# Kernel tuning notes

Measured on AMD Instinct MI355X. Metric: run time of the kernel, lower is better.

Reference implementation:

```python
import jax, jax.numpy as jnp
import numpy as np

B, IN_DIM, OUT_DIM = 4096, 8192, 8192

# Each of the 16 gates op_i(a,b) is affine in (1, a, b, a*b).
# Rows: [const, coef_a, coef_b, coef_ab] for gate i = 0..15.
GATE_COEF = np.array([
    [0.,  0.,  0.,  0.],   # 0: zeros
    [0.,  0.,  0.,  1.],   # 1: a*b
    [0.,  1.,  0., -1.],   # 2: a - a*b
    [0.,  1.,  0.,  0.],   # 3: a
    [0.,  0.,  1., -1.],   # 4: b - a*b
    [0.,  0.,  1.,  0.],   # 5: b
    [0.,  1.,  1., -2.],   # 6: a + b - 2ab (xor)
    [0.,  1.,  1., -1.],   # 7: a + b - ab (or)
    [1., -1., -1.,  1.],   # 8: 1 - (a + b - ab)
    [1., -1., -1.,  2.],   # 9: 1 - (a + b - 2ab)
    [1.,  0., -1.,  0.],   # 10: 1 - b
    [1.,  0., -1.,  1.],   # 11: 1 - b + ab
    [1., -1.,  0.,  0.],   # 12: 1 - a
    [1., -1.,  0.,  1.],   # 13: 1 - a + ab
    [1.,  0.,  0., -1.],   # 14: 1 - ab
    [1.,  0.,  0.,  0.],   # 15: ones
], dtype=np.float32)


def setup_inputs() -> dict:
    key = jax.random.key(0)
    k1, k2, k3, k4 = jax.random.split(key, 4)
    x = jax.random.uniform(k1, (B, IN_DIM), dtype=jnp.float32)
    weights = jax.random.normal(k2, (OUT_DIM, 16), dtype=jnp.float32)
    idx0 = jax.random.randint(k3, (OUT_DIM,), 0, IN_DIM)
    idx1 = jax.random.randint(k4, (OUT_DIM,), 0, IN_DIM)
    return {"x": x, "weights": weights, "idx0": idx0, "idx1": idx1}


def reference(x, weights, idx0, idx1):
    # training path: soft mixture over 16 gates
    p = jax.nn.softmax(weights, axis=-1)          # [out_dim, 16]
    c = p @ jnp.asarray(GATE_COEF)                # [out_dim, 4]: sum_i p_i * op_i collapsed
    a = x[:, idx0]                                # [B, out_dim]
    b = x[:, idx1]                                # [B, out_dim]
    return c[:, 0] + c[:, 1] * a + c[:, 2] * b + c[:, 3] * (a * b)
```

## Files before the change

kernel.cpp:

```cpp
#include <hip/hip_runtime.h>

#define IN_DIM 8192
#define OUT_DIM 8192
#define NROWS 4096
#define THREADS 512
#define JITERS (OUT_DIM / (THREADS * 4))

__device__ __constant__ float GATE_COEF[16][4] = {
    {0.f, 0.f, 0.f, 0.f}, {0.f, 0.f, 0.f, 1.f}, {0.f, 1.f, 0.f, -1.f}, {0.f, 1.f, 0.f, 0.f},
    {0.f, 0.f, 1.f, -1.f}, {0.f, 0.f, 1.f, 0.f}, {0.f, 1.f, 1.f, -2.f}, {0.f, 1.f, 1.f, -1.f},
    {1.f, -1.f, -1.f, 1.f}, {1.f, -1.f, -1.f, 2.f}, {1.f, 0.f, -1.f, 0.f}, {1.f, 0.f, -1.f, 1.f},
    {1.f, -1.f, 0.f, 0.f}, {1.f, -1.f, 0.f, 1.f}, {1.f, 0.f, 0.f, -1.f}, {1.f, 0.f, 0.f, 0.f}};

__global__ __launch_bounds__(256) void compute_c_kernel(const float* __restrict__ w,
                                                        float4* __restrict__ c) {
    int j = blockIdx.x * blockDim.x + threadIdx.x;
    if (j >= OUT_DIM) return;
    const float4* wv = (const float4*)(w + (size_t)j * 16);
    float4 w0 = wv[0], w1 = wv[1], w2 = wv[2], w3 = wv[3];
    float wa[16] = {w0.x, w0.y, w0.z, w0.w, w1.x, w1.y, w1.z, w1.w,
                    w2.x, w2.y, w2.z, w2.w, w3.x, w3.y, w3.z, w3.w};
    float m = wa[0];
#pragma unroll
    for (int k = 1; k < 16; ++k) m = fmaxf(m, wa[k]);
    float p[16];
    float s = 0.f;
#pragma unroll
    for (int k = 0; k < 16; ++k) {
        p[k] = __expf(wa[k] - m);
        s += p[k];
    }
    float inv = 1.f / s;
    float c0 = 0.f, c1 = 0.f, c2 = 0.f, c3 = 0.f;
#pragma unroll
    for (int k = 0; k < 16; ++k) {
        c0 = fmaf(p[k], GATE_COEF[k][0], c0);
        c1 = fmaf(p[k], GATE_COEF[k][1], c1);
        c2 = fmaf(p[k], GATE_COEF[k][2], c2);
        c3 = fmaf(p[k], GATE_COEF[k][3], c3);
    }
    c[j] = make_float4(c0 * inv, c1 * inv, c2 * inv, c3 * inv);
}

__global__ __launch_bounds__(THREADS, 8) void gate_kernel(const float* __restrict__ x,
                                                          const float4* __restrict__ c,
                                                          const int* __restrict__ idx0,
                                                          const int* __restrict__ idx1,
                                                          float* __restrict__ out) {
    __shared__ float row[IN_DIM];
    const int i = blockIdx.x;
    const int tid = threadIdx.x;
    const float4* xr = (const float4*)(x + (size_t)i * IN_DIM);
    float4* rowv = (float4*)row;

    float4 s0 = xr[tid];
    float4 s1 = xr[tid + THREADS];
    float4 s2 = xr[tid + 2 * THREADS];
    float4 s3 = xr[tid + 3 * THREADS];

    const int j0 = tid * 4;
    int4 pi0 = *(const int4*)(idx0 + j0);
    int4 pi1 = *(const int4*)(idx1 + j0);

    rowv[tid] = s0;
    rowv[tid + THREADS] = s1;
    rowv[tid + 2 * THREADS] = s2;
    rowv[tid + 3 * THREADS] = s3;
    __syncthreads();

    float* orow = out + (size_t)i * OUT_DIM;
#pragma unroll
    for (int k = 0; k < JITERS; ++k) {
        const int j = k * (THREADS * 4) + tid * 4;
        const int4 i0 = pi0;
        const int4 i1 = pi1;
        if (k < JITERS - 1) {
            const int jn = j + THREADS * 4;
            pi0 = *(const int4*)(idx0 + jn);
            pi1 = *(const int4*)(idx1 + jn);
        }
        const float4 ca = c[j + 0];
        const float4 cb = c[j + 1];
        const float4 cc = c[j + 2];
        const float4 cd = c[j + 3];
        float a, b;
        float4 o;
        a = row[i0.x]; b = row[i1.x];
        o.x = fmaf(a * b, ca.w, fmaf(b, ca.z, fmaf(a, ca.y, ca.x)));
        a = row[i0.y]; b = row[i1.y];
        o.y = fmaf(a * b, cb.w, fmaf(b, cb.z, fmaf(a, cb.y, cb.x)));
        a = row[i0.z]; b = row[i1.z];
        o.z = fmaf(a * b, cc.w, fmaf(b, cc.z, fmaf(a, cc.y, cc.x)));
        a = row[i0.w]; b = row[i1.w];
        o.w = fmaf(a * b, cd.w, fmaf(b, cd.z, fmaf(a, cd.y, cd.x)));
        *(float4*)(orow + j) = o;
    }
}

extern "C" void kernel_launch(void* const* d_in, const int* in_sizes, int n_in,
                              void* d_out, int out_size, void* d_ws, size_t ws_size,
                              hipStream_t stream) {
    const float* x = (const float*)d_in[0];
    const float* weights = (const float*)d_in[1];
    const int* idx0 = (const int*)d_in[2];
    const int* idx1 = (const int*)d_in[3];
    float* out = (float*)d_out;
    float4* c = (float4*)d_ws;

    compute_c_kernel<<<OUT_DIM / 256, 256, 0, stream>>>(weights, c);
    gate_kernel<<<NROWS, THREADS, 0, stream>>>(x, c, idx0, idx1, out);
}
```

Measured before the change: 277.6 us.

## Process two rows per block, use SoA coefficients and nontemporal loads/stores

Each block now stages two x rows in shared memory (64KB) and reuses the index and coefficient loads for both rows. The coefficients are stored structure-of-arrays so each thread reads four coalesced float4 vectors instead of four scattered float4 per output. Loads of x and stores of out use nontemporal hints to avoid polluting cache. The doubled LDS footprint lowers the number of resident blocks per CU, which may reduce latency hiding.

```diff
diff --git a/kernel.cpp b/kernel.cpp
--- a/kernel.cpp
+++ b/kernel.cpp
@@ -4,7 +4,10 @@
 #define OUT_DIM 8192
 #define NROWS 4096
 #define THREADS 512
+#define RPB 2
 #define JITERS (OUT_DIM / (THREADS * 4))
+
+typedef float v4f __attribute__((ext_vector_type(4)));
 
 __device__ __constant__ float GATE_COEF[16][4] = {
     {0.f, 0.f, 0.f, 0.f}, {0.f, 0.f, 0.f, 1.f}, {0.f, 1.f, 0.f, -1.f}, {0.f, 1.f, 0.f, 0.f},
@@ -13,7 +16,7 @@
     {1.f, -1.f, 0.f, 0.f}, {1.f, -1.f, 0.f, 1.f}, {1.f, 0.f, 0.f, -1.f}, {1.f, 0.f, 0.f, 0.f}};
 
 __global__ __launch_bounds__(256) void compute_c_kernel(const float* __restrict__ w,
-                                                        float4* __restrict__ c) {
+                                                        float* __restrict__ cp) {
     int j = blockIdx.x * blockDim.x + threadIdx.x;
     if (j >= OUT_DIM) return;
     const float4* wv = (const float4*)(w + (size_t)j * 16);
@@ -39,36 +42,48 @@
         c2 = fmaf(p[k], GATE_COEF[k][2], c2);
         c3 = fmaf(p[k], GATE_COEF[k][3], c3);
     }
-    c[j] = make_float4(c0 * inv, c1 * inv, c2 * inv, c3 * inv);
+    cp[j] = c0 * inv;
+    cp[j + OUT_DIM] = c1 * inv;
+    cp[j + 2 * OUT_DIM] = c2 * inv;
+    cp[j + 3 * OUT_DIM] = c3 * inv;
 }
 
-__global__ __launch_bounds__(THREADS, 8) void gate_kernel(const float* __restrict__ x,
-                                                          const float4* __restrict__ c,
+__global__ __launch_bounds__(THREADS, 4) void gate_kernel(const float* __restrict__ x,
+                                                          const float* __restrict__ cp,
                                                           const int* __restrict__ idx0,
                                                           const int* __restrict__ idx1,
                                                           float* __restrict__ out) {
-    __shared__ float row[IN_DIM];
-    const int i = blockIdx.x;
+    __shared__ float rows[RPB * IN_DIM];
+    const int r0 = blockIdx.x * RPB;
     const int tid = threadIdx.x;
-    const float4* xr = (const float4*)(x + (size_t)i * IN_DIM);
-    float4* rowv = (float4*)row;
 
-    float4 s0 = xr[tid];
-    float4 s1 = xr[tid + THREADS];
-    float4 s2 = xr[tid + 2 * THREADS];
-    float4 s3 = xr[tid + 3 * THREADS];
+    const v4f* xr0 = (const v4f*)(x + (size_t)r0 * IN_DIM);
+    const v4f* xr1 = (const v4f*)(x + (size_t)(r0 + 1) * IN_DIM);
+    v4f* rv0 = (v4f*)rows;
+    v4f* rv1 = (v4f*)(rows + IN_DIM);
+    v4f st[8];
+#pragma unroll
+    for (int t = 0; t < 4; ++t) st[t] = __builtin_nontemporal_load(xr0 + tid + t * THREADS);
+#pragma unroll
+    for (int t = 0; t < 4; ++t) st[4 + t] = __builtin_nontemporal_load(xr1 + tid + t * THREADS);
 
     const int j0 = tid * 4;
     int4 pi0 = *(const int4*)(idx0 + j0);
     int4 pi1 = *(const int4*)(idx1 + j0);
 
-    rowv[tid] = s0;
-    rowv[tid + THREADS] = s1;
-    rowv[tid + 2 * THREADS] = s2;
-    rowv[tid + 3 * THREADS] = s3;
+#pragma unroll
+    for (int t = 0; t < 4; ++t) rv0[tid + t * THREADS] = st[t];
+#pragma unroll
+    for (int t = 0; t < 4; ++t) rv1[tid + t * THREADS] = st[4 + t];
     __syncthreads();
 
-    float* orow = out + (size_t)i * OUT_DIM;
+    const float* __restrict__ c0p = cp;
+    const float* __restrict__ c1p = cp + OUT_DIM;
+    const float* __restrict__ c2p = cp + 2 * OUT_DIM;
+    const float* __restrict__ c3p = cp + 3 * OUT_DIM;
+    float* o0 = out + (size_t)r0 * OUT_DIM;
+    float* o1 = out + (size_t)(r0 + 1) * OUT_DIM;
+
 #pragma unroll
     for (int k = 0; k < JITERS; ++k) {
         const int j = k * (THREADS * 4) + tid * 4;
@@ -79,21 +94,22 @@
             pi0 = *(const int4*)(idx0 + jn);
             pi1 = *(const int4*)(idx1 + jn);
         }
-        const float4 ca = c[j + 0];
-        const float4 cb = c[j + 1];
-        const float4 cc = c[j + 2];
-        const float4 cd = c[j + 3];
-        float a, b;
-        float4 o;
-        a = row[i0.x]; b = row[i1.x];
-        o.x = fmaf(a * b, ca.w, fmaf(b, ca.z, fmaf(a, ca.y, ca.x)));
-        a = row[i0.y]; b = row[i1.y];
-        o.y = fmaf(a * b, cb.w, fmaf(b, cb.z, fmaf(a, cb.y, cb.x)));
-        a = row[i0.z]; b = row[i1.z];
-        o.z = fmaf(a * b, cc.w, fmaf(b, cc.z, fmaf(a, cc.y, cc.x)));
-        a = row[i0.w]; b = row[i1.w];
-        o.w = fmaf(a * b, cd.w, fmaf(b, cd.z, fmaf(a, cd.y, cd.x)));
-        *(float4*)(orow + j) = o;
+        const v4f c0v = *(const v4f*)(c0p + j);
+        const v4f c1v = *(const v4f*)(c1p + j);
+        const v4f c2v = *(const v4f*)(c2p + j);
+        const v4f c3v = *(const v4f*)(c3p + j);
+        v4f a0, b0, a1, b1;
+        a0.x = rows[i0.x]; a0.y = rows[i0.y]; a0.z = rows[i0.z]; a0.w = rows[i0.w];
+        b0.x = rows[i1.x]; b0.y = rows[i1.y]; b0.z = rows[i1.z]; b0.w = rows[i1.w];
+        a1.x = rows[IN_DIM + i0.x]; a1.y = rows[IN_DIM + i0.y];
+        a1.z = rows[IN_DIM + i0.z]; a1.w = rows[IN_DIM + i0.w];
+        b1.x = rows[IN_DIM + i1.x]; b1.y = rows[IN_DIM + i1.y];
+        b1.z = rows[IN_DIM + i1.z]; b1.w = rows[IN_DIM + i1.w];
+
+        const v4f r0v = c0v + c1v * a0 + c2v * b0 + c3v * (a0 * b0);
+        const v4f r1v = c0v + c1v * a1 + c2v * b1 + c3v * (a1 * b1);
+        __builtin_nontemporal_store(r0v, (v4f*)(o0 + j));
+        __builtin_nontemporal_store(r1v, (v4f*)(o1 + j));
     }
 }
 
@@ -105,8 +121,8 @@
     const int* idx0 = (const int*)d_in[2];
     const int* idx1 = (const int*)d_in[3];
     float* out = (float*)d_out;
-    float4* c = (float4*)d_ws;
+    float* cp = (float*)d_ws;
 
-    compute_c_kernel<<<OUT_DIM / 256, 256, 0, stream>>>(weights, c);
-    gate_kernel<<<NROWS, THREADS, 0, stream>>>(x, c, idx0, idx1, out);
+    compute_c_kernel<<<OUT_DIM / 256, 256, 0, stream>>>(weights, cp);
+    gate_kernel<<<NROWS / RPB, THREADS, 0, stream>>>(x, cp, idx0, idx1, out);
 }
```

After: 234.8 us. 15.4% less time.
